# Kernel optimization log

Measured on AMD Instinct MI355X. Metric: run time of the kernel, lower is better.

Reference implementation:

```python
import jax, jax.numpy as jnp
import numpy as np

TAU = 2.0   # membrane time constant
V_TH = 0.5  # firing threshold

@jax.custom_vjp
def spike_fn(v):
    return jnp.where(v > 0, 1.0, 0.0)

def _spike_fwd(v):
    return spike_fn(v), v

def _spike_bwd(v, g):
    # atan surrogate gradient (alpha=2): d s / d v = 1 / (1 + (pi*v)^2)
    sg = 1.0 / (1.0 + (jnp.pi * v) ** 2)
    return (g * sg,)

spike_fn.defvjp(_spike_fwd, _spike_bwd)


def setup_inputs() -> dict:
    key = jax.random.key(0)
    # [batch, neurons, time] -- time on axis 2, matching moveaxis(x, 2, 0)
    x = jax.random.normal(key, (32, 16384, 100), dtype=jnp.float32)
    return {"x": x}


def reference(x):
    x_seq = jnp.moveaxis(x, 2, 0)  # [T, B, N]
    decay = 1.0 - 1.0 / TAU

    def scan_fn(v, x_t):
        v = v * decay + x_t            # leaky integrate
        s = spike_fn(v - V_TH)         # fire
        v = v - s * V_TH               # soft reset
        return v, s

    v_init = jnp.zeros_like(x_seq[0])
    _, spikes = jax.lax.scan(scan_fn, v_init, x_seq)
    return jnp.moveaxis(spikes, 0, 2)  # [B, N, T]
```

## Files before the change

kernel.cpp:

```cpp
#include <hip/hip_runtime.h>


#define T_STEPS 100
#define T_VEC   25
#define ROWS    32
#define BF4     (ROWS * T_VEC)
#define NDMA    13
#define NST     13
#define DECAY   0.5f
#define VTH     0.5f

typedef float vfloat4 __attribute__((ext_vector_type(4)));

__device__ __forceinline__ void gll16(const vfloat4* g, vfloat4* l) {
    __builtin_amdgcn_global_load_lds(
        (const __attribute__((address_space(1))) void*)g,
        (__attribute__((address_space(3))) void*)l, 16, 0, 0);
}

__global__ __launch_bounds__(64) void lif_gll32(const float* __restrict__ x,
                                                float* __restrict__ out,
                                                int n_rows) {
    __shared__ vfloat4 tile[BF4];
    __shared__ uint4   bits[ROWS];

    const int lane = threadIdx.x;
    const long long row0 = (long long)blockIdx.x * ROWS;
    const long long gf0  = row0 * T_VEC;
    const long long total_f4 = (long long)n_rows * T_VEC;

    const vfloat4* __restrict__ xb = reinterpret_cast<const vfloat4*>(x);

    #pragma unroll
    for (int k = 0; k < NDMA; ++k) {
        int f = k * 64 + lane;
        if (f < BF4 && gf0 + f < total_f4)
            gll16(xb + (gf0 + f), &tile[k * 64]);
    }

    asm volatile("s_waitcnt vmcnt(0)" ::: "memory");
    __builtin_amdgcn_sched_barrier(0);

    if (lane < ROWS && row0 + lane < n_rows) {
        unsigned int pk0 = 0, pk1 = 0, pk2 = 0, pk3 = 0;
        float v = 0.0f;
        #pragma unroll
        for (int c = 0; c < T_VEC; ++c) {
            vfloat4 xs = tile[lane * T_VEC + c];
            #pragma unroll
            for (int k = 0; k < 4; ++k) {
                v = v * DECAY + xs[k];
                bool sp = (v - VTH > 0.0f);
                v -= sp ? VTH : 0.0f;
                unsigned int bit = sp ? 1u : 0u;
                const int b = c * 4 + k;
                if      (b < 32) pk0 |= bit << b;
                else if (b < 64) pk1 |= bit << (b - 32);
                else if (b < 96) pk2 |= bit << (b - 64);
                else             pk3 |= bit << (b - 96);
            }
        }
        uint4 w; w.x = pk0; w.y = pk1; w.z = pk2; w.w = pk3;
        bits[lane] = w;
    }
    __syncthreads();

    vfloat4* __restrict__ ob = reinterpret_cast<vfloat4*>(out);
    const unsigned int* bw = reinterpret_cast<const unsigned int*>(bits);
    #pragma unroll
    for (int i = 0; i < NST; ++i) {
        int f = i * 64 + lane;
        long long g = gf0 + f;
        if (f < BF4 && g < total_f4) {
            int r  = f / T_VEC;
            int c4 = f % T_VEC;
            unsigned int word = bw[r * 4 + (c4 >> 3)];
            unsigned int nib = (word >> ((c4 & 7) * 4)) & 0xFu;
            vfloat4 s;
            s.x = (nib & 1u) ? 1.0f : 0.0f;
            s.y = (nib & 2u) ? 1.0f : 0.0f;
            s.z = (nib & 4u) ? 1.0f : 0.0f;
            s.w = (nib & 8u) ? 1.0f : 0.0f;
            ob[g] = s;
        }
    }
}

extern "C" void kernel_launch(void* const* d_in, const int* in_sizes, int n_in,
                              void* d_out, int out_size, void* d_ws, size_t ws_size,
                              hipStream_t stream) {
    const float* x = (const float*)d_in[0];
    float* out = (float*)d_out;

    int n_rows = in_sizes[0] / T_STEPS;
    int grid = (n_rows + ROWS - 1) / ROWS;

    lif_gll32<<<grid, 64, 0, stream>>>(x, out, n_rows);
}
```

Measured before the change: 82.44 us.

## Split block tile into two halves to overlap second load with first compute

Each block's 32 rows are split into two 16-row halves loaded into separate LDS buffers. A partial vmcnt wait lets the first half be computed and stored while the second half's global-to-LDS loads are still in flight. The __syncthreads between the bit-packing and the store phase is replaced by sched_barrier. That is only safe because the block is a single 64-thread wavefront. The risk is that vmcnt counting is thrown off by predicated-off loads, and by the first half's stores before the second wait, which makes the synchronisation fragile.

```diff
diff --git a/kernel.cpp b/kernel.cpp
--- a/kernel.cpp
+++ b/kernel.cpp
@@ -4,9 +4,9 @@
 #define T_STEPS 100
 #define T_VEC   25
 #define ROWS    32
-#define BF4     (ROWS * T_VEC)
-#define NDMA    13
-#define NST     13
+#define HR      16
+#define HF4     (HR * T_VEC)
+#define NDMA    7
 #define DECAY   0.5f
 #define VTH     0.5f
 
@@ -18,35 +18,43 @@
         (__attribute__((address_space(3))) void*)l, 16, 0, 0);
 }
 
-__global__ __launch_bounds__(64) void lif_gll32(const float* __restrict__ x,
+__global__ __launch_bounds__(64) void lif_gll2h(const float* __restrict__ x,
                                                 float* __restrict__ out,
                                                 int n_rows) {
-    __shared__ vfloat4 tile[BF4];
-    __shared__ uint4   bits[ROWS];
+    __shared__ vfloat4 tileA[HF4];
+    __shared__ vfloat4 tileB[HF4];
+    __shared__ uint4   bits[HR];
 
     const int lane = threadIdx.x;
     const long long row0 = (long long)blockIdx.x * ROWS;
     const long long gf0  = row0 * T_VEC;
+    const long long gf1  = gf0 + HF4;
     const long long total_f4 = (long long)n_rows * T_VEC;
 
     const vfloat4* __restrict__ xb = reinterpret_cast<const vfloat4*>(x);
+    vfloat4* __restrict__ ob       = reinterpret_cast<vfloat4*>(out);
+    const unsigned int* bw = reinterpret_cast<const unsigned int*>(bits);
 
     #pragma unroll
     for (int k = 0; k < NDMA; ++k) {
         int f = k * 64 + lane;
-        if (f < BF4 && gf0 + f < total_f4)
-            gll16(xb + (gf0 + f), &tile[k * 64]);
+        if (f < HF4 && gf0 + f < total_f4) gll16(xb + (gf0 + f), &tileA[k * 64]);
     }
-
-    asm volatile("s_waitcnt vmcnt(0)" ::: "memory");
+    #pragma unroll
+    for (int k = 0; k < NDMA; ++k) {
+        int f = k * 64 + lane;
+        if (f < HF4 && gf1 + f < total_f4) gll16(xb + (gf1 + f), &tileB[k * 64]);
+    }
+    __builtin_amdgcn_sched_barrier(0);
+    asm volatile("s_waitcnt vmcnt(7)" ::: "memory");
     __builtin_amdgcn_sched_barrier(0);
 
-    if (lane < ROWS && row0 + lane < n_rows) {
+    if (lane < HR && row0 + lane < n_rows) {
         unsigned int pk0 = 0, pk1 = 0, pk2 = 0, pk3 = 0;
         float v = 0.0f;
         #pragma unroll
         for (int c = 0; c < T_VEC; ++c) {
-            vfloat4 xs = tile[lane * T_VEC + c];
+            vfloat4 xs = tileA[lane * T_VEC + c];
             #pragma unroll
             for (int k = 0; k < 4; ++k) {
                 v = v * DECAY + xs[k];
@@ -63,15 +71,58 @@
         uint4 w; w.x = pk0; w.y = pk1; w.z = pk2; w.w = pk3;
         bits[lane] = w;
     }
-    __syncthreads();
+    __builtin_amdgcn_sched_barrier(0);
 
-    vfloat4* __restrict__ ob = reinterpret_cast<vfloat4*>(out);
-    const unsigned int* bw = reinterpret_cast<const unsigned int*>(bits);
     #pragma unroll
-    for (int i = 0; i < NST; ++i) {
+    for (int i = 0; i < NDMA; ++i) {
         int f = i * 64 + lane;
         long long g = gf0 + f;
-        if (f < BF4 && g < total_f4) {
+        if (f < HF4 && g < total_f4) {
+            int r  = f / T_VEC;
+            int c4 = f % T_VEC;
+            unsigned int word = bw[r * 4 + (c4 >> 3)];
+            unsigned int nib = (word >> ((c4 & 7) * 4)) & 0xFu;
+            vfloat4 s;
+            s.x = (nib & 1u) ? 1.0f : 0.0f;
+            s.y = (nib & 2u) ? 1.0f : 0.0f;
+            s.z = (nib & 4u) ? 1.0f : 0.0f;
+            s.w = (nib & 8u) ? 1.0f : 0.0f;
+            ob[g] = s;
+        }
+    }
+    __builtin_amdgcn_sched_barrier(0);
+    asm volatile("s_waitcnt vmcnt(7)" ::: "memory");
+    __builtin_amdgcn_sched_barrier(0);
+
+    if (lane < HR && row0 + HR + lane < n_rows) {
+        unsigned int pk0 = 0, pk1 = 0, pk2 = 0, pk3 = 0;
+        float v = 0.0f;
+        #pragma unroll
+        for (int c = 0; c < T_VEC; ++c) {
+            vfloat4 xs = tileB[lane * T_VEC + c];
+            #pragma unroll
+            for (int k = 0; k < 4; ++k) {
+                v = v * DECAY + xs[k];
+                bool sp = (v - VTH > 0.0f);
+                v -= sp ? VTH : 0.0f;
+                unsigned int bit = sp ? 1u : 0u;
+                const int b = c * 4 + k;
+                if      (b < 32) pk0 |= bit << b;
+                else if (b < 64) pk1 |= bit << (b - 32);
+                else if (b < 96) pk2 |= bit << (b - 64);
+                else             pk3 |= bit << (b - 96);
+            }
+        }
+        uint4 w; w.x = pk0; w.y = pk1; w.z = pk2; w.w = pk3;
+        bits[lane] = w;
+    }
+    __builtin_amdgcn_sched_barrier(0);
+
+    #pragma unroll
+    for (int i = 0; i < NDMA; ++i) {
+        int f = i * 64 + lane;
+        long long g = gf1 + f;
+        if (f < HF4 && g < total_f4) {
             int r  = f / T_VEC;
             int c4 = f % T_VEC;
             unsigned int word = bw[r * 4 + (c4 >> 3)];
@@ -95,5 +146,5 @@
     int n_rows = in_sizes[0] / T_STEPS;
     int grid = (n_rows + ROWS - 1) / ROWS;
 
-    lif_gll32<<<grid, 64, 0, stream>>>(x, out, n_rows);
+    lif_gll2h<<<grid, 64, 0, stream>>>(x, out, n_rows);
 }
```

Result: slower. 84.94 us (+3.0%).
